# Kernel optimization log

Measured on AMD Instinct MI355X. Metric: run time of the kernel, lower is better.

Reference implementation:

```python
import jax, jax.numpy as jnp
import numpy as np

B, T, F, H, D1, D2, OUT = 8192, 90, 7, 128, 128, 64, 30


def _layernorm(x, g, b, eps=1e-5):
    mu = jnp.mean(x, axis=-1, keepdims=True)
    var = jnp.mean((x - mu) ** 2, axis=-1, keepdims=True)
    return (x - mu) * jax.lax.rsqrt(var + eps) * g + b


def _lstm_layer(x, Wih, Whh, bih, bhh):
    # x: [B,T,H_in]; Wih: [4H,H_in]; Whh: [4H,H]; biases [4H]. PyTorch gate order i,f,g,o.
    xg = jnp.einsum('bti,gi->btg', x, Wih) + bih + bhh  # [B,T,4H] precomputed input projection
    xg_t = jnp.swapaxes(xg, 0, 1)  # [T,B,4H]

    def step(carry, gx):
        h, c = carry
        gates = gx + h @ Whh.T  # [B,4H]
        i, f, g, o = jnp.split(gates, 4, axis=-1)
        c = jax.nn.sigmoid(f) * c + jax.nn.sigmoid(i) * jnp.tanh(g)
        h = jax.nn.sigmoid(o) * jnp.tanh(c)
        return (h, c), h

    h0 = jnp.zeros((x.shape[0], H), x.dtype)
    (_, _), hs = jax.lax.scan(step, (h0, h0), xg_t)
    return jnp.swapaxes(hs, 0, 1)  # [B,T,H]


def setup_inputs() -> dict:
    key = jax.random.key(0)
    ks = jax.random.split(key, 16)
    s = lambda k, shape, scale: jax.random.normal(k, shape, jnp.float32) * scale
    inp = {
        'x': s(ks[0], (B, T, F), 1.0),
        'W_in': s(ks[1], (H, F), 0.3), 'b_in': jnp.zeros((H,)),
        'g_in': jnp.ones((H,)), 'be_in': jnp.zeros((H,)),
        'Wih0': s(ks[2], (4 * H, H), 0.08), 'Whh0': s(ks[3], (4 * H, H), 0.08),
        'bih0': jnp.zeros((4 * H,)).at[H:2 * H].set(1.0), 'bhh0': jnp.zeros((4 * H,)),
        'Wih1': s(ks[4], (4 * H, H), 0.08), 'Whh1': s(ks[5], (4 * H, H), 0.08),
        'bih1': jnp.zeros((4 * H,)).at[H:2 * H].set(1.0), 'bhh1': jnp.zeros((4 * H,)),
        'g_ln': jnp.ones((H,)), 'be_ln': jnp.zeros((H,)),
        'W_d1': s(ks[6], (D1, H), 0.12), 'b_d1': jnp.zeros((D1,)),
        'W_d2': s(ks[7], (D2, D1), 0.12), 'b_d2': jnp.zeros((D2,)),
        'W_d3': s(ks[8], (OUT, D2), 0.15), 'b_d3': jnp.zeros((OUT,)),
    }
    return inp


def reference(x, W_in, b_in, g_in, be_in,
              Wih0, Whh0, bih0, bhh0, Wih1, Whh1, bih1, bhh1,
              g_ln, be_ln, W_d1, b_d1, W_d2, b_d2, W_d3, b_d3):
    h = _layernorm(jnp.einsum('btf,hf->bth', x, W_in) + b_in, g_in, be_in)
    h = _lstm_layer(h, Wih0, Whh0, bih0, bhh0)
    h = _lstm_layer(h, Wih1, Whh1, bih1, bhh1)  # dropout between layers is eval no-op
    last = _layernorm(h[:, -1, :], g_ln, be_ln)  # [B,H]
    d = jax.nn.relu(last @ W_d1.T + b_d1)
    d = jax.nn.relu(d @ W_d2.T + b_d2)
    return d @ W_d3.T + b_d3  # [B,30]
```

## Files before the change

### kernel.cpp

```cpp
#include <hip/hip_runtime.h>

#define DEV __device__ __forceinline__
typedef unsigned short u16;
typedef unsigned int u32;
typedef __bf16 bf16x8 __attribute__((ext_vector_type(8)));
typedef float f32x4 __attribute__((ext_vector_type(4)));

static constexpr int B = 8192, T = 90, F = 7, H = 128, NOUT = 30;

DEV float fexp2(float x) { return __builtin_amdgcn_exp2f(x); }
DEV float frcp(float x) { return __builtin_amdgcn_rcpf(x); }
DEV float frsq(float x) { return __builtin_amdgcn_rsqf(x); }
DEV float sigm(float x) { return frcp(1.f + fexp2(-1.44269504088896341f * x)); }
DEV u16 f2bfbits(float f) { __bf16 b = (__bf16)f; return __builtin_bit_cast(u16, b); }
DEV float bfbits2f(u32 u) { return __builtin_bit_cast(float, u << 16); }
DEV u32 pk2(float a, float b) { return (u32)f2bfbits(a) | ((u32)f2bfbits(b) << 16); }

DEV float wave_sum(float v) {
#pragma unroll
    for (int m = 32; m; m >>= 1) v += __shfl_xor(v, m, 64);
    return v;
}

__global__ __launch_bounds__(512) void prep_aux(
    const float* __restrict__ W_in, const float* __restrict__ b_in,
    const float* __restrict__ g_in, const float* __restrict__ be_in,
    const float* __restrict__ Wih0, float* __restrict__ aux, u16* __restrict__ Uhat) {
    const int tid = threadIdx.x;
    if (tid < 7) {
        float sm = 0.f, sp = 0.f;
        for (int h = 0; h < 128; ++h) { const float w = W_in[h * 7 + tid]; sm += w; sp += w * b_in[h]; }
        aux[tid] = sm * (1.f / 128.f); aux[64 + tid] = sp * (1.f / 128.f);
    } else if (tid < 56) {
        const int cd = tid - 7, cc = cd / 7, dd = cd % 7;
        float s = 0.f;
        for (int h = 0; h < 128; ++h) s += W_in[h * 7 + cc] * W_in[h * 7 + dd];
        aux[8 + cd] = s * (1.f / 128.f);
    } else if (tid == 56) {
        float s = 0.f; for (int h = 0; h < 128; ++h) s += b_in[h];
        aux[7] = s * (1.f / 128.f);
    } else if (tid == 57) {
        float s = 0.f; for (int h = 0; h < 128; ++h) s += b_in[h] * b_in[h];
        aux[72] = s * (1.f / 128.f);
    }
    float acc[10];
#pragma unroll
    for (int i = 0; i < 10; ++i) acc[i] = 0.f;
    const float* wr = Wih0 + (long)tid * 128;
    for (int h = 0; h < 128; ++h) {
        const float wv = wr[h], wg = wv * g_in[h];
#pragma unroll
        for (int cc = 0; cc < 7; ++cc) acc[cc] += wg * W_in[h * 7 + cc];
        acc[7] += wg * b_in[h]; acc[8] += wg; acc[9] += wv * be_in[h];
    }
    u16* dst = Uhat + tid * 32;
#pragma unroll
    for (int cc = 0; cc < 10; ++cc) dst[cc] = f2bfbits(acc[cc]);
#pragma unroll
    for (int cc = 10; cc < 32; ++cc) dst[cc] = 0;
}

__global__ __launch_bounds__(256) void prep_stats(
    const float* __restrict__ x, const float* __restrict__ aux,
    float2* __restrict__ stats) {
    __shared__ float sa[80];
    const int tid = threadIdx.x;
    if (tid < 80) sa[tid] = aux[tid];
    __syncthreads();
    const long idx = (long)blockIdx.x * 256 + tid;
    const float* xr = x + idx * 7;
    float xv[7];
#pragma unroll
    for (int cc = 0; cc < 7; ++cc) xv[cc] = xr[cc];
    float mu = sa[7];
#pragma unroll
    for (int cc = 0; cc < 7; ++cc) mu += sa[cc] * xv[cc];
    float q = sa[72];
#pragma unroll
    for (int cc = 0; cc < 7; ++cc) {
        float tacc = 2.f * sa[64 + cc];
#pragma unroll
        for (int dd = 0; dd < 7; ++dd) tacc += sa[8 + cc * 7 + dd] * xv[dd];
        q += xv[cc] * tacc;
    }
    const float rstd = frsq(q - mu * mu + 1e-5f);
    stats[idx] = make_float2(rstd, -rstd * mu);
}

__global__ __launch_bounds__(512, 2) void lstm_rec_l1(
    const float* __restrict__ x, const float2* __restrict__ stats,
    const u16* __restrict__ Uhat, const float* __restrict__ Whh,
    const float* __restrict__ bih, const float* __restrict__ bhh,
    u16* __restrict__ hs) {
    __shared__ __align__(16) u16 s_z[2][2][4][16][8];
    __shared__ __align__(16) u16 s_h[2][2][16 * 128];

    const int tid = threadIdx.x;
    const int wave = tid >> 6, lane = tid & 63, quad = lane >> 4, n16 = lane & 15;
    const int b0 = blockIdx.x * 32;

    for (int i = tid; i < 2 * 2 * 4 * 16 * 8; i += 512) ((u16*)s_z)[i] = 0;
    for (int i = tid; i < 2 * 16 * 128; i += 512) ((u16*)s_h[1])[i] = 0;

    bf16x8 bU[4], bWhh[4][4];
    float bias[4];
#pragma unroll
    for (int g = 0; g < 4; ++g) {
        const int wrow = g * 128 + 16 * wave + n16;
        bias[g] = bih[wrow] + bhh[wrow];
        bU[g] = *(const bf16x8*)&Uhat[wrow * 32 + quad * 8];
#pragma unroll
        for (int kk = 0; kk < 4; ++kk) {
            const float* ph = Whh + (long)wrow * 128 + kk * 32 + quad * 8;
            bf16x8 bh;
#pragma unroll
            for (int j = 0; j < 8; ++j) bh[j] = (__bf16)ph[j];
            bWhh[g][kk] = bh;
        }
    }

    const f32x4 zero4 = {0.f, 0.f, 0.f, 0.f};
    float c[2][4];
#pragma unroll
    for (int mt = 0; mt < 2; ++mt)
#pragma unroll
        for (int r = 0; r < 4; ++r) c[mt][r] = 0.f;

    const bool stager = (lane < 8);
    const int tau = wave * 8 + lane;
    const int srow = tau & 31, skk8 = tau >> 5;
    const int smt = srow >> 4, sm = srow & 15;
    const long srowg = (long)(b0 + srow) * T;

    const int ftile = tid >> 8, finner = tid & 255;
    const int fm = finner & 15, fkk8 = finner >> 4;
    const int fldsoff = (fkk8 * 16 + fm) * 8;
    const size_t fgrow = (size_t)(b0 + ftile * 16 + fm) * T;
    const int fgcol = fkk8 * 8;

    __syncthreads();

    if (stager) {
        const float2 st0 = stats[srowg];
        u32 p0, p1, p2, p3;
        if (skk8 == 0) {
            const float* xp = x + srowg * 7;
            const float rs = st0.x;
            p0 = pk2(rs * xp[0], rs * xp[1]); p1 = pk2(rs * xp[2], rs * xp[3]);
            p2 = pk2(rs * xp[4], rs * xp[5]); p3 = pk2(rs * xp[6], rs);
        } else { p0 = pk2(st0.y, 1.f); p1 = 0; p2 = 0; p3 = 0; }
        *(uint4*)&s_z[0][smt][skk8][sm][0] = (uint4){p0, p1, p2, p3};
    }
    __syncthreads();

#pragma unroll 1
    for (int t = 0; t < T; ++t) {
        const int par = t & 1;
        const int t1 = t + 1;
        const bool hasPre = stager && (t1 < T);
        float2 nst = {};
        float nx[7];
        if (hasPre) {
            nst = stats[srowg + t1];
            if (skk8 == 0) {
                const float* xp = x + (srowg + t1) * 7;
#pragma unroll
                for (int j = 0; j < 7; ++j) nx[j] = xp[j];
            }
        }
        if (t > 0) {
            const uint4 hv = *(const uint4*)&s_h[par ^ 1][ftile][fldsoff];
            *(uint4*)(hs + (fgrow + (t - 1)) * 128 + fgcol) = hv;
        }

#pragma unroll
        for (int mt = 0; mt < 2; ++mt) {
            const bf16x8 az = *(const bf16x8*)&s_z[par][mt][quad][n16][0];
            bf16x8 ah[4];
#pragma unroll
            for (int kk = 0; kk < 4; ++kk)
                ah[kk] = *(const bf16x8*)&s_h[par ^ 1][mt][((kk * 4 + quad) * 16 + n16) * 8];
            f32x4 acc[4];
#pragma unroll
            for (int g = 0; g < 4; ++g) {
                f32x4 a = __builtin_amdgcn_mfma_f32_16x16x32_bf16(az, bU[g], zero4, 0, 0, 0);
#pragma unroll
                for (int kk = 0; kk < 4; ++kk)
                    a = __builtin_amdgcn_mfma_f32_16x16x32_bf16(ah[kk], bWhh[g][kk], a, 0, 0, 0);
                acc[g] = a;
            }
#pragma unroll
            for (int r = 0; r < 4; ++r) {
                const float xi = acc[0][r] + bias[0];
                const float xf = acc[1][r] + bias[1];
                const float xg = acc[2][r] + bias[2];
                const float xo = acc[3][r] + bias[3];
                const float tg = 2.f * frcp(1.f + fexp2(-2.88539008177792681f * xg)) - 1.f;
                const float cn = sigm(xf) * c[mt][r] + sigm(xi) * tg;
                c[mt][r] = cn;
                const float so = sigm(xo);
                const float rr = frcp(1.f + fexp2(-2.88539008177792681f * cn));
                const float hv = __builtin_fmaf(2.f * so, rr, -so);
                s_h[par][mt][((2 * wave + (n16 >> 3)) * 16 + (quad * 4 + r)) * 8 + (n16 & 7)] =
                    f2bfbits(hv);
            }
        }

        if (hasPre) {
            u32 p0, p1, p2, p3;
            if (skk8 == 0) {
                const float rs = nst.x;
                p0 = pk2(rs * nx[0], rs * nx[1]); p1 = pk2(rs * nx[2], rs * nx[3]);
                p2 = pk2(rs * nx[4], rs * nx[5]); p3 = pk2(rs * nx[6], rs);
            } else { p0 = pk2(nst.y, 1.f); p1 = 0; p2 = 0; p3 = 0; }
            *(uint4*)&s_z[par ^ 1][smt][skk8][sm][0] = (uint4){p0, p1, p2, p3};
        }
        __syncthreads();
    }
    {
        const uint4 hv = *(const uint4*)&s_h[1][ftile][fldsoff];
        *(uint4*)(hs + (fgrow + (T - 1)) * 128 + fgcol) = hv;
    }
}

__global__ __launch_bounds__(512, 2) void lstm_rec_l2(
    const float* __restrict__ Wih, const float* __restrict__ Whh,
    const float* __restrict__ bih, const float* __restrict__ bhh,
    const u16* __restrict__ xin, u16* __restrict__ hlast) {
    __shared__ __align__(16) u16 s_x[2][2][16 * 128];
    __shared__ __align__(16) u16 s_h[2][2][16 * 128];

    const int tid = threadIdx.x;
    const int wave = tid >> 6, lane = tid & 63, quad = lane >> 4, n16 = lane & 15;
    const int b0 = blockIdx.x * 32;

    for (int i = tid; i < 2 * 16 * 128; i += 512) ((u16*)s_h[1])[i] = 0;

    bf16x8 bWih[4][4], bWhh[4][4];
    float bias[4];
#pragma unroll
    for (int g = 0; g < 4; ++g) {
        const int wrow = g * 128 + 16 * wave + n16;
        bias[g] = bih[wrow] + bhh[wrow];
#pragma unroll
        for (int kk = 0; kk < 4; ++kk) {
            const float* pi = Wih + (long)wrow * 128 + kk * 32 + quad * 8;
            const float* ph = Whh + (long)wrow * 128 + kk * 32 + quad * 8;
            bf16x8 bi, bh;
#pragma unroll
            for (int j = 0; j < 8; ++j) { bi[j] = (__bf16)pi[j]; bh[j] = (__bf16)ph[j]; }
            bWih[g][kk] = bi; bWhh[g][kk] = bh;
        }
    }

    const f32x4 zero4 = {0.f, 0.f, 0.f, 0.f};
    float c[2][4];
#pragma unroll
    for (int mt = 0; mt < 2; ++mt)
#pragma unroll
        for (int r = 0; r < 4; ++r) c[mt][r] = 0.f;

    const int stile = tid >> 8, sinner = tid & 255;
    const int sm = sinner & 15, skk8 = sinner >> 4;
    const u16* gsrc = xin + (size_t)(b0 + stile * 16 + sm) * T * 128 + skk8 * 8;
    const int ftile = tid >> 8, finner = tid & 255;
    const int fm = finner & 15, fkk8 = finner >> 4;
    const int fldsoff = (fkk8 * 16 + fm) * 8;
    const int fgcol = fkk8 * 8;

    {
        const uint4 v = *(const uint4*)gsrc;
        *(uint4*)&s_x[0][stile][sinner * 8] = v;
    }
    __syncthreads();

#pragma unroll 1
    for (int t = 0; t < T; ++t) {
        const int par = t & 1;
        uint4 pre = {};
        const bool hasPre = (t + 1 < T);
        if (hasPre) pre = *(const uint4*)(gsrc + (size_t)(t + 1) * 128);

#pragma unroll
        for (int mt = 0; mt < 2; ++mt) {
            bf16x8 aln[4], ah[4];
#pragma unroll
            for (int kk = 0; kk < 4; ++kk) {
                aln[kk] = *(const bf16x8*)&s_x[par][mt][((kk * 4 + quad) * 16 + n16) * 8];
                ah[kk] = *(const bf16x8*)&s_h[par ^ 1][mt][((kk * 4 + quad) * 16 + n16) * 8];
            }
            f32x4 acc[4];
#pragma unroll
            for (int g = 0; g < 4; ++g) {
                f32x4 a = __builtin_amdgcn_mfma_f32_16x16x32_bf16(aln[0], bWih[g][0], zero4, 0, 0, 0);
                a = __builtin_amdgcn_mfma_f32_16x16x32_bf16(ah[0], bWhh[g][0], a, 0, 0, 0);
#pragma unroll
                for (int kk = 1; kk < 4; ++kk) {
                    a = __builtin_amdgcn_mfma_f32_16x16x32_bf16(aln[kk], bWih[g][kk], a, 0, 0, 0);
                    a = __builtin_amdgcn_mfma_f32_16x16x32_bf16(ah[kk], bWhh[g][kk], a, 0, 0, 0);
                }
                acc[g] = a;
            }
#pragma unroll
            for (int r = 0; r < 4; ++r) {
                const float xi = acc[0][r] + bias[0];
                const float xf = acc[1][r] + bias[1];
                const float xg = acc[2][r] + bias[2];
                const float xo = acc[3][r] + bias[3];
                const float tg = 2.f * frcp(1.f + fexp2(-2.88539008177792681f * xg)) - 1.f;
                const float cn = sigm(xf) * c[mt][r] + sigm(xi) * tg;
                c[mt][r] = cn;
                const float so = sigm(xo);
                const float rr = frcp(1.f + fexp2(-2.88539008177792681f * cn));
                const float hv = __builtin_fmaf(2.f * so, rr, -so);
                s_h[par][mt][((2 * wave + (n16 >> 3)) * 16 + (quad * 4 + r)) * 8 + (n16 & 7)] =
                    f2bfbits(hv);
            }
        }
        if (hasPre) *(uint4*)&s_x[par ^ 1][stile][sinner * 8] = pre;
        __syncthreads();
    }
    {
        const uint4 hv = *(const uint4*)&s_h[1][ftile][fldsoff];
        *(uint4*)(hlast + (size_t)(b0 + ftile * 16 + fm) * 128 + fgcol) = hv;
    }
}

__global__ __launch_bounds__(256) void dense_head(
    const u16* __restrict__ hlast, const float* __restrict__ g_ln,
    const float* __restrict__ be_ln, const float* __restrict__ W_d1,
    const float* __restrict__ b_d1, const float* __restrict__ W_d2,
    const float* __restrict__ b_d2, const float* __restrict__ W_d3,
    const float* __restrict__ b_d3, float* __restrict__ out) {
    __shared__ float s_ln[16][128];
    __shared__ float s_d1[16][128];
    __shared__ float s_d2[16][64];
    const int wave = threadIdx.x >> 6, lane = threadIdx.x & 63;
    const long base = (long)blockIdx.x * 16;
    const int R = wave * 4;

#pragma unroll
    for (int rr = 0; rr < 4; ++rr) {
        const long row = base + R + rr;
        const u32 packed = ((const u32*)hlast)[row * 64 + lane];
        float v0 = bfbits2f(packed & 0xffffu), v1 = bfbits2f(packed >> 16);
        const float s = wave_sum(v0 + v1);
        const float q = wave_sum(v0 * v0 + v1 * v1);
        const float mu = s * (1.f / 128.f);
        const float rstd = frsq(q * (1.f / 128.f) - mu * mu + 1e-5f);
        const int h0 = 2 * lane;
        s_ln[R + rr][h0] = (v0 - mu) * rstd * g_ln[h0] + be_ln[h0];
        s_ln[R + rr][h0 + 1] = (v1 - mu) * rstd * g_ln[h0 + 1] + be_ln[h0 + 1];
    }
    __syncthreads();

#pragma unroll
    for (int half = 0; half < 2; ++half) {
        const int o = lane + 64 * half;
        float a[4] = {b_d1[o], b_d1[o], b_d1[o], b_d1[o]};
        const float4* wr = (const float4*)(W_d1 + (long)o * 128);
#pragma unroll 8
        for (int k = 0; k < 32; ++k) {
            const float4 wv = wr[k];
#pragma unroll
            for (int rr = 0; rr < 4; ++rr) {
                const float4 xv = ((const float4*)s_ln[R + rr])[k];
                a[rr] += wv.x * xv.x + wv.y * xv.y + wv.z * xv.z + wv.w * xv.w;
            }
        }
#pragma unroll
        for (int rr = 0; rr < 4; ++rr) s_d1[R + rr][o] = fmaxf(a[rr], 0.f);
    }
    __syncthreads();

    {
        float a[4] = {b_d2[lane], b_d2[lane], b_d2[lane], b_d2[lane]};
        const float4* wr = (const float4*)(W_d2 + (long)lane * 128);
#pragma unroll 8
        for (int k = 0; k < 32; ++k) {
            const float4 wv = wr[k];
#pragma unroll
            for (int rr = 0; rr < 4; ++rr) {
                const float4 xv = ((const float4*)s_d1[R + rr])[k];
                a[rr] += wv.x * xv.x + wv.y * xv.y + wv.z * xv.z + wv.w * xv.w;
            }
        }
#pragma unroll
        for (int rr = 0; rr < 4; ++rr) s_d2[R + rr][lane] = fmaxf(a[rr], 0.f);
    }
    __syncthreads();

    if (lane < NOUT) {
        float a[4] = {b_d3[lane], b_d3[lane], b_d3[lane], b_d3[lane]};
        const float4* wr = (const float4*)(W_d3 + (long)lane * 64);
#pragma unroll
        for (int k = 0; k < 16; ++k) {
            const float4 wv = wr[k];
#pragma unroll
            for (int rr = 0; rr < 4; ++rr) {
                const float4 xv = ((const float4*)s_d2[R + rr])[k];
                a[rr] += wv.x * xv.x + wv.y * xv.y + wv.z * xv.z + wv.w * xv.w;
            }
        }
#pragma unroll
        for (int rr = 0; rr < 4; ++rr) out[(base + R + rr) * NOUT + lane] = a[rr];
    }
}

extern "C" void kernel_launch(void* const* d_in, const int* in_sizes, int n_in,
                              void* d_out, int out_size, void* d_ws, size_t ws_size,
                              hipStream_t stream) {
    const float* x = (const float*)d_in[0];
    const float* W_in = (const float*)d_in[1];
    const float* b_in = (const float*)d_in[2];
    const float* g_in = (const float*)d_in[3];
    const float* be_in = (const float*)d_in[4];
    const float* Wih0 = (const float*)d_in[5];
    const float* Whh0 = (const float*)d_in[6];
    const float* bih0 = (const float*)d_in[7];
    const float* bhh0 = (const float*)d_in[8];
    const float* Wih1 = (const float*)d_in[9];
    const float* Whh1 = (const float*)d_in[10];
    const float* bih1 = (const float*)d_in[11];
    const float* bhh1 = (const float*)d_in[12];
    const float* g_ln = (const float*)d_in[13];
    const float* be_ln = (const float*)d_in[14];
    const float* W_d1 = (const float*)d_in[15];
    const float* b_d1 = (const float*)d_in[16];
    const float* W_d2 = (const float*)d_in[17];
    const float* b_d2 = (const float*)d_in[18];
    const float* W_d3 = (const float*)d_in[19];
    const float* b_d3 = (const float*)d_in[20];
    float* out = (float*)d_out;

    char* w = (char*)d_ws;
    float* aux = (float*)w;               w += 512;
    u16* Uhat = (u16*)w;                  w += 512 * 32 * sizeof(u16);
    float2* stats = (float2*)w;           w += (size_t)B * T * sizeof(float2);
    u16* hs0 = (u16*)w;                   w += (size_t)B * T * H * sizeof(u16);
    u16* hlast = (u16*)w;

    prep_aux<<<1, 512, 0, stream>>>(W_in, b_in, g_in, be_in, Wih0, aux, Uhat);
    prep_stats<<<(B * T) / 256, 256, 0, stream>>>(x, aux, stats);
    lstm_rec_l1<<<B / 32, 512, 0, stream>>>(x, stats, Uhat, Whh0, bih0, bhh0, hs0);
    lstm_rec_l2<<<B / 32, 512, 0, stream>>>(Wih1, Whh1, bih1, bhh1, hs0, hlast);
    dense_head<<<B / 16, 256, 0, stream>>>(hlast, g_ln, be_ln, W_d1, b_d1, W_d2, b_d2,
                                           W_d3, b_d3, out);
}
```

Measured before the change: 554.3 us.

## Interleave two batch tiles to overlap gate math with MFMA in LSTM recurrences

Both LSTM recurrence kernels now process the two 16-row batch tiles in a staggered way. The gate nonlinearities of one tile run while the MFMAs of the other tile issue, with a triple-buffered input stage and a barrier per half-step. The bias is folded into the MFMA accumulator init. A new cvt3 kernel pre-converts the recurrent and input weights to bf16 once, so each block no longer converts fp32 weights itself. The cost is one extra launch, more live registers under a 2-blocks-per-CU launch bound, and twice as many __syncthreads per timestep.

```diff
diff --git a/kernel.cpp b/kernel.cpp
--- a/kernel.cpp
+++ b/kernel.cpp
@@ -60,6 +60,18 @@
     for (int cc = 10; cc < 32; ++cc) dst[cc] = 0;
 }
 
+__global__ __launch_bounds__(256) void cvt3(
+    const float* __restrict__ a, const float* __restrict__ b,
+    const float* __restrict__ c, u16* __restrict__ dst) {
+    const long i = (long)blockIdx.x * 256 + threadIdx.x;
+    const int which = (int)(i >> 14);
+    const long off = (i & 16383) * 4;
+    const float* src = which == 0 ? a : (which == 1 ? b : c);
+    const float4 v = *(const float4*)(src + off);
+    u32 p0 = pk2(v.x, v.y), p1 = pk2(v.z, v.w);
+    *(uint2*)(dst + (long)which * 65536 + off) = (uint2){p0, p1};
+}
+
 __global__ __launch_bounds__(256) void prep_stats(
     const float* __restrict__ x, const float* __restrict__ aux,
     float2* __restrict__ stats) {
@@ -89,240 +101,243 @@
 
 __global__ __launch_bounds__(512, 2) void lstm_rec_l1(
     const float* __restrict__ x, const float2* __restrict__ stats,
-    const u16* __restrict__ Uhat, const float* __restrict__ Whh,
+    const u16* __restrict__ Uhat, const u16* __restrict__ Whhb,
     const float* __restrict__ bih, const float* __restrict__ bhh,
     u16* __restrict__ hs) {
-    __shared__ __align__(16) u16 s_z[2][2][4][16][8];
-    __shared__ __align__(16) u16 s_h[2][2][16 * 128];
+    __shared__ __align__(16) u16 s_z[2][3][4][16][8];
+    __shared__ __align__(16) u16 s_h[2][2][2048];
 
     const int tid = threadIdx.x;
     const int wave = tid >> 6, lane = tid & 63, quad = lane >> 4, n16 = lane & 15;
     const int b0 = blockIdx.x * 32;
 
-    for (int i = tid; i < 2 * 2 * 4 * 16 * 8; i += 512) ((u16*)s_z)[i] = 0;
-    for (int i = tid; i < 2 * 16 * 128; i += 512) ((u16*)s_h[1])[i] = 0;
+    for (int i = tid; i < 2 * 3 * 4 * 16 * 8; i += 512) ((u16*)s_z)[i] = 0;
+    for (int i = tid; i < 2048; i += 512) { s_h[0][1][i] = 0; s_h[1][1][i] = 0; }
 
     bf16x8 bU[4], bWhh[4][4];
-    float bias[4];
+    f32x4 bias4[4];
 #pragma unroll
     for (int g = 0; g < 4; ++g) {
         const int wrow = g * 128 + 16 * wave + n16;
-        bias[g] = bih[wrow] + bhh[wrow];
+        const float bb = bih[wrow] + bhh[wrow];
+        bias4[g] = (f32x4){bb, bb, bb, bb};
         bU[g] = *(const bf16x8*)&Uhat[wrow * 32 + quad * 8];
 #pragma unroll
-        for (int kk = 0; kk < 4; ++kk) {
-            const float* ph = Whh + (long)wrow * 128 + kk * 32 + quad * 8;
-            bf16x8 bh;
-#pragma unroll
-            for (int j = 0; j < 8; ++j) bh[j] = (__bf16)ph[j];
-            bWhh[g][kk] = bh;
-        }
-    }
-
-    const f32x4 zero4 = {0.f, 0.f, 0.f, 0.f};
-    float c[2][4];
-#pragma unroll
-    for (int mt = 0; mt < 2; ++mt)
-#pragma unroll
-        for (int r = 0; r < 4; ++r) c[mt][r] = 0.f;
-
-    const bool stager = (lane < 8);
-    const int tau = wave * 8 + lane;
-    const int srow = tau & 31, skk8 = tau >> 5;
-    const int smt = srow >> 4, sm = srow & 15;
-    const long srowg = (long)(b0 + srow) * T;
-
-    const int ftile = tid >> 8, finner = tid & 255;
-    const int fm = finner & 15, fkk8 = finner >> 4;
-    const int fldsoff = (fkk8 * 16 + fm) * 8;
-    const size_t fgrow = (size_t)(b0 + ftile * 16 + fm) * T;
-    const int fgcol = fkk8 * 8;
-
-    __syncthreads();
-
-    if (stager) {
-        const float2 st0 = stats[srowg];
+        for (int kk = 0; kk < 4; ++kk)
+            bWhh[g][kk] = *(const bf16x8*)&Whhb[(long)wrow * 128 + kk * 32 + quad * 8];
+    }
+
+    const bool zst = (tid < 32);
+    const int srow = tid & 15, skk8z = tid >> 4;
+    const bool stg = (tid < 256);
+    const int fm = tid & 15, fkk8 = (tid >> 4) & 15;
+    const int fldso = (fkk8 * 16 + fm) * 8;
+
+    auto build_z = [&](size_t sidx, u16* dst) {
+        const float2 st = stats[sidx];
         u32 p0, p1, p2, p3;
-        if (skk8 == 0) {
-            const float* xp = x + srowg * 7;
-            const float rs = st0.x;
+        if (skk8z == 0) {
+            const float* xp = x + sidx * 7;
+            const float rs = st.x;
             p0 = pk2(rs * xp[0], rs * xp[1]); p1 = pk2(rs * xp[2], rs * xp[3]);
             p2 = pk2(rs * xp[4], rs * xp[5]); p3 = pk2(rs * xp[6], rs);
-        } else { p0 = pk2(st0.y, 1.f); p1 = 0; p2 = 0; p3 = 0; }
-        *(uint4*)&s_z[0][smt][skk8][sm][0] = (uint4){p0, p1, p2, p3};
-    }
-    __syncthreads();
+        } else { p0 = pk2(st.y, 1.f); p1 = 0; p2 = 0; p3 = 0; }
+        *(uint4*)dst = (uint4){p0, p1, p2, p3};
+    };
+
+    __syncthreads();
+
+    if (zst) {
+#pragma unroll
+        for (int tl = 0; tl < 2; ++tl)
+#pragma unroll
+            for (int tt = 0; tt < 2; ++tt)
+                build_z((size_t)(b0 + tl * 16 + srow) * T + tt, &s_z[tl][tt][skk8z][srow][0]);
+    }
+    __syncthreads();
+
+    auto do_mfma = [&](const u16* szb, const u16* shb, f32x4* gcn) {
+        const bf16x8 az = *(const bf16x8*)&szb[(quad * 16 + n16) * 8];
+        bf16x8 ah[4];
+#pragma unroll
+        for (int kk = 0; kk < 4; ++kk)
+            ah[kk] = *(const bf16x8*)&shb[((kk * 4 + quad) * 16 + n16) * 8];
+#pragma unroll
+        for (int g = 0; g < 4; ++g) {
+            f32x4 a = __builtin_amdgcn_mfma_f32_16x16x32_bf16(az, bU[g], bias4[g], 0, 0, 0);
+#pragma unroll
+            for (int kk = 0; kk < 4; ++kk)
+                a = __builtin_amdgcn_mfma_f32_16x16x32_bf16(ah[kk], bWhh[g][kk], a, 0, 0, 0);
+            gcn[g] = a;
+        }
+    };
+    auto do_gates = [&](const f32x4* gco, float* cc, u16* shout) {
+#pragma unroll
+        for (int r = 0; r < 4; ++r) {
+            const float xi = gco[0][r], xf = gco[1][r], xgg = gco[2][r], xo = gco[3][r];
+            const float tg = 2.f * frcp(1.f + fexp2(-2.88539008177792681f * xgg)) - 1.f;
+            const float cn = sigm(xf) * cc[r] + sigm(xi) * tg;
+            cc[r] = cn;
+            const float so = sigm(xo);
+            const float rr = frcp(1.f + fexp2(-2.88539008177792681f * cn));
+            const float hv = __builtin_fmaf(2.f * so, rr, -so);
+            shout[((2 * wave + (n16 >> 3)) * 16 + (quad * 4 + r)) * 8 + (n16 & 7)] = f2bfbits(hv);
+        }
+    };
+
+    float cA[4] = {0.f, 0.f, 0.f, 0.f}, cB[4] = {0.f, 0.f, 0.f, 0.f};
+    f32x4 gc[4], gn[4];
 
 #pragma unroll 1
-    for (int t = 0; t < T; ++t) {
-        const int par = t & 1;
-        const int t1 = t + 1;
-        const bool hasPre = stager && (t1 < T);
-        float2 nst = {};
-        float nx[7];
-        if (hasPre) {
-            nst = stats[srowg + t1];
-            if (skk8 == 0) {
-                const float* xp = x + (srowg + t1) * 7;
-#pragma unroll
-                for (int j = 0; j < 7; ++j) nx[j] = xp[j];
-            }
-        }
-        if (t > 0) {
-            const uint4 hv = *(const uint4*)&s_h[par ^ 1][ftile][fldsoff];
-            *(uint4*)(hs + (fgrow + (t - 1)) * 128 + fgcol) = hv;
-        }
-
-#pragma unroll
-        for (int mt = 0; mt < 2; ++mt) {
-            const bf16x8 az = *(const bf16x8*)&s_z[par][mt][quad][n16][0];
-            bf16x8 ah[4];
-#pragma unroll
-            for (int kk = 0; kk < 4; ++kk)
-                ah[kk] = *(const bf16x8*)&s_h[par ^ 1][mt][((kk * 4 + quad) * 16 + n16) * 8];
-            f32x4 acc[4];
-#pragma unroll
-            for (int g = 0; g < 4; ++g) {
-                f32x4 a = __builtin_amdgcn_mfma_f32_16x16x32_bf16(az, bU[g], zero4, 0, 0, 0);
-#pragma unroll
-                for (int kk = 0; kk < 4; ++kk)
-                    a = __builtin_amdgcn_mfma_f32_16x16x32_bf16(ah[kk], bWhh[g][kk], a, 0, 0, 0);
-                acc[g] = a;
-            }
-#pragma unroll
-            for (int r = 0; r < 4; ++r) {
-                const float xi = acc[0][r] + bias[0];
-                const float xf = acc[1][r] + bias[1];
-                const float xg = acc[2][r] + bias[2];
-                const float xo = acc[3][r] + bias[3];
-                const float tg = 2.f * frcp(1.f + fexp2(-2.88539008177792681f * xg)) - 1.f;
-                const float cn = sigm(xf) * c[mt][r] + sigm(xi) * tg;
-                c[mt][r] = cn;
-                const float so = sigm(xo);
-                const float rr = frcp(1.f + fexp2(-2.88539008177792681f * cn));
-                const float hv = __builtin_fmaf(2.f * so, rr, -so);
-                s_h[par][mt][((2 * wave + (n16 >> 3)) * 16 + (quad * 4 + r)) * 8 + (n16 & 7)] =
-                    f2bfbits(hv);
-            }
-        }
-
-        if (hasPre) {
-            u32 p0, p1, p2, p3;
-            if (skk8 == 0) {
-                const float rs = nst.x;
-                p0 = pk2(rs * nx[0], rs * nx[1]); p1 = pk2(rs * nx[2], rs * nx[3]);
-                p2 = pk2(rs * nx[4], rs * nx[5]); p3 = pk2(rs * nx[6], rs);
-            } else { p0 = pk2(nst.y, 1.f); p1 = 0; p2 = 0; p3 = 0; }
-            *(uint4*)&s_z[par ^ 1][smt][skk8][sm][0] = (uint4){p0, p1, p2, p3};
-        }
+    for (int t2 = 0; t2 < T; ++t2) {
+        const int tm = t2 % 3;
+        const int tw = (tm >= 1) ? tm - 1 : tm + 2;
+        const int ph = t2 & 1, pho = ph ^ 1;
+        const bool hasPre = (t2 + 2 < T);
+
+        do_mfma(&s_z[0][tm][0][0][0], s_h[0][pho], gn);
+        if (t2 > 0 && stg) {
+            const uint4 hv = *(const uint4*)&s_h[0][pho][fldso];
+            *(uint4*)(hs + ((size_t)(b0 + fm) * T + (t2 - 1)) * 128 + fkk8 * 8) = hv;
+        }
+        if (t2 > 0) do_gates(gc, cB, s_h[1][pho]);
+#pragma unroll
+        for (int g = 0; g < 4; ++g) gc[g] = gn[g];
+        if (hasPre && zst)
+            build_z((size_t)(b0 + srow) * T + t2 + 2, &s_z[0][tw][skk8z][srow][0]);
         __syncthreads();
-    }
-    {
-        const uint4 hv = *(const uint4*)&s_h[1][ftile][fldsoff];
-        *(uint4*)(hs + (fgrow + (T - 1)) * 128 + fgcol) = hv;
+
+        do_mfma(&s_z[1][tm][0][0][0], s_h[1][pho], gn);
+        if (t2 > 0 && stg) {
+            const uint4 hv = *(const uint4*)&s_h[1][pho][fldso];
+            *(uint4*)(hs + ((size_t)(b0 + 16 + fm) * T + (t2 - 1)) * 128 + fkk8 * 8) = hv;
+        }
+        do_gates(gc, cA, s_h[0][ph]);
+#pragma unroll
+        for (int g = 0; g < 4; ++g) gc[g] = gn[g];
+        if (hasPre && zst)
+            build_z((size_t)(b0 + 16 + srow) * T + t2 + 2, &s_z[1][tw][skk8z][srow][0]);
+        __syncthreads();
+    }
+    do_gates(gc, cB, s_h[1][1]);
+    __syncthreads();
+    if (stg) {
+        const uint4 hvA = *(const uint4*)&s_h[0][1][fldso];
+        const uint4 hvB = *(const uint4*)&s_h[1][1][fldso];
+        *(uint4*)(hs + ((size_t)(b0 + fm) * T + (T - 1)) * 128 + fkk8 * 8) = hvA;
+        *(uint4*)(hs + ((size_t)(b0 + 16 + fm) * T + (T - 1)) * 128 + fkk8 * 8) = hvB;
     }
 }
 
 __global__ __launch_bounds__(512, 2) void lstm_rec_l2(
-    const float* __restrict__ Wih, const float* __restrict__ Whh,
+    const u16* __restrict__ Wihb, const u16* __restrict__ Whhb,
     const float* __restrict__ bih, const float* __restrict__ bhh,
     const u16* __restrict__ xin, u16* __restrict__ hlast) {
-    __shared__ __align__(16) u16 s_x[2][2][16 * 128];
-    __shared__ __align__(16) u16 s_h[2][2][16 * 128];
+    __shared__ __align__(16) u16 s_x[2][3][2048];
+    __shared__ __align__(16) u16 s_h[2][2][2048];
 
     const int tid = threadIdx.x;
     const int wave = tid >> 6, lane = tid & 63, quad = lane >> 4, n16 = lane & 15;
     const int b0 = blockIdx.x * 32;
 
-    for (int i = tid; i < 2 * 16 * 128; i += 512) ((u16*)s_h[1])[i] = 0;
+    for (int i = tid; i < 2048; i += 512) { s_h[0][1][i] = 0; s_h[1][1][i] = 0; }
 
     bf16x8 bWih[4][4], bWhh[4][4];
-    float bias[4];
+    f32x4 bias4[4];
 #pragma unroll
     for (int g = 0; g < 4; ++g) {
         const int wrow = g * 128 + 16 * wave + n16;
-        bias[g] = bih[wrow] + bhh[wrow];
+        const float bb = bih[wrow] + bhh[wrow];
+        bias4[g] = (f32x4){bb, bb, bb, bb};
 #pragma unroll
         for (int kk = 0; kk < 4; ++kk) {
-            const float* pi = Wih + (long)wrow * 128 + kk * 32 + quad * 8;
-            const float* ph = Whh + (long)wrow * 128 + kk * 32 + quad * 8;
-            bf16x8 bi, bh;
-#pragma unroll
-            for (int j = 0; j < 8; ++j) { bi[j] = (__bf16)pi[j]; bh[j] = (__bf16)ph[j]; }
-            bWih[g][kk] = bi; bWhh[g][kk] = bh;
-        }
-    }
-
-    const f32x4 zero4 = {0.f, 0.f, 0.f, 0.f};
-    float c[2][4];
-#pragma unroll
-    for (int mt = 0; mt < 2; ++mt)
-#pragma unroll
-        for (int r = 0; r < 4; ++r) c[mt][r] = 0.f;
-
-    const int stile = tid >> 8, sinner = tid & 255;
-    const int sm = sinner & 15, skk8 = sinner >> 4;
-    const u16* gsrc = xin + (size_t)(b0 + stile * 16 + sm) * T * 128 + skk8 * 8;
-    const int ftile = tid >> 8, finner = tid & 255;
-    const int fm = finner & 15, fkk8 = finner >> 4;
-    const int fldsoff = (fkk8 * 16 + fm) * 8;
-    const int fgcol = fkk8 * 8;
-
-    {
-        const uint4 v = *(const uint4*)gsrc;
-        *(uint4*)&s_x[0][stile][sinner * 8] = v;
-    }
-    __syncthreads();
+            bWih[g][kk] = *(const bf16x8*)&Wihb[(long)wrow * 128 + kk * 32 + quad * 8];
+            bWhh[g][kk] = *(const bf16x8*)&Whhb[(long)wrow * 128 + kk * 32 + quad * 8];
+        }
+    }
+
+    const bool stg = (tid < 256);
+    const int fm = tid & 15, fkk8 = (tid >> 4) & 15;
+    const int fldso = (fkk8 * 16 + fm) * 8;
+    const u16* gsA = xin + (size_t)(b0 + fm) * T * 128 + fkk8 * 8;
+    const u16* gsB = xin + (size_t)(b0 + 16 + fm) * T * 128 + fkk8 * 8;
+
+    if (stg) {
+#pragma unroll
+        for (int tt = 0; tt < 2; ++tt) {
+            *(uint4*)&s_x[0][tt][fldso] = *(const uint4*)(gsA + (size_t)tt * 128);
+            *(uint4*)&s_x[1][tt][fldso] = *(const uint4*)(gsB + (size_t)tt * 128);
+        }
+    }
+    __syncthreads();
+
+    auto do_mfma = [&](const u16* sxb, const u16* shb, f32x4* gcn) {
+        bf16x8 ax[4], ah[4];
+#pragma unroll
+        for (int kk = 0; kk < 4; ++kk) {
+            ax[kk] = *(const bf16x8*)&sxb[((kk * 4 + quad) * 16 + n16) * 8];
+            ah[kk] = *(const bf16x8*)&shb[((kk * 4 + quad) * 16 + n16) * 8];
+        }
+#pragma unroll
+        for (int g = 0; g < 4; ++g) {
+            f32x4 a = bias4[g];
+#pragma unroll
+            for (int kk = 0; kk < 4; ++kk) {
+                a = __builtin_amdgcn_mfma_f32_16x16x32_bf16(ax[kk], bWih[g][kk], a, 0, 0, 0);
+                a = __builtin_amdgcn_mfma_f32_16x16x32_bf16(ah[kk], bWhh[g][kk], a, 0, 0, 0);
+            }
+            gcn[g] = a;
+        }
+    };
+    auto do_gates = [&](const f32x4* gco, float* cc, u16* shout) {
+#pragma unroll
+        for (int r = 0; r < 4; ++r) {
+            const float xi = gco[0][r], xf = gco[1][r], xgg = gco[2][r], xo = gco[3][r];
+            const float tg = 2.f * frcp(1.f + fexp2(-2.88539008177792681f * xgg)) - 1.f;
+            const float cn = sigm(xf) * cc[r] + sigm(xi) * tg;
+            cc[r] = cn;
+            const float so = sigm(xo);
+            const float rr = frcp(1.f + fexp2(-2.88539008177792681f * cn));
+            const float hv = __builtin_fmaf(2.f * so, rr, -so);
+            shout[((2 * wave + (n16 >> 3)) * 16 + (quad * 4 + r)) * 8 + (n16 & 7)] = f2bfbits(hv);
+        }
+    };
+
+    float cA[4] = {0.f, 0.f, 0.f, 0.f}, cB[4] = {0.f, 0.f, 0.f, 0.f};
+    f32x4 gc[4], gn[4];
 
 #pragma unroll 1
-    for (int t = 0; t < T; ++t) {
-        const int par = t & 1;
-        uint4 pre = {};
-        const bool hasPre = (t + 1 < T);
-        if (hasPre) pre = *(const uint4*)(gsrc + (size_t)(t + 1) * 128);
-
-#pragma unroll
-        for (int mt = 0; mt < 2; ++mt) {
-            bf16x8 aln[4], ah[4];
-#pragma unroll
-            for (int kk = 0; kk < 4; ++kk) {
-                aln[kk] = *(const bf16x8*)&s_x[par][mt][((kk * 4 + quad) * 16 + n16) * 8];
-                ah[kk] = *(const bf16x8*)&s_h[par ^ 1][mt][((kk * 4 + quad) * 16 + n16) * 8];
-            }
-            f32x4 acc[4];
-#pragma unroll
-            for (int g = 0; g < 4; ++g) {
-                f32x4 a = __builtin_amdgcn_mfma_f32_16x16x32_bf16(aln[0], bWih[g][0], zero4, 0, 0, 0);
-                a = __builtin_amdgcn_mfma_f32_16x16x32_bf16(ah[0], bWhh[g][0], a, 0, 0, 0);
-#pragma unroll
-                for (int kk = 1; kk < 4; ++kk) {
-                    a = __builtin_amdgcn_mfma_f32_16x16x32_bf16(aln[kk], bWih[g][kk], a, 0, 0, 0);
-                    a = __builtin_amdgcn_mfma_f32_16x16x32_bf16(ah[kk], bWhh[g][kk], a, 0, 0, 0);
-                }
-                acc[g] = a;
-            }
-#pragma unroll
-            for (int r = 0; r < 4; ++r) {
-                const float xi = acc[0][r] + bias[0];
-                const float xf = acc[1][r] + bias[1];
-                const float xg = acc[2][r] + bias[2];
-                const float xo = acc[3][r] + bias[3];
-                const float tg = 2.f * frcp(1.f + fexp2(-2.88539008177792681f * xg)) - 1.f;
-                const float cn = sigm(xf) * c[mt][r] + sigm(xi) * tg;
-                c[mt][r] = cn;
-                const float so = sigm(xo);
-                const float rr = frcp(1.f + fexp2(-2.88539008177792681f * cn));
-                const float hv = __builtin_fmaf(2.f * so, rr, -so);
-                s_h[par][mt][((2 * wave + (n16 >> 3)) * 16 + (quad * 4 + r)) * 8 + (n16 & 7)] =
-                    f2bfbits(hv);
-            }
-        }
-        if (hasPre) *(uint4*)&s_x[par ^ 1][stile][sinner * 8] = pre;
+    for (int t2 = 0; t2 < T; ++t2) {
+        const int tm = t2 % 3;
+        const int tw = (tm >= 1) ? tm - 1 : tm + 2;
+        const int ph = t2 & 1, pho = ph ^ 1;
+        const bool hasPre = (t2 + 2 < T);
+
+        uint4 preA = {};
+        if (hasPre && stg) preA = *(const uint4*)(gsA + (size_t)(t2 + 2) * 128);
+        do_mfma(s_x[0][tm], s_h[0][pho], gn);
+        if (t2 > 0) do_gates(gc, cB, s_h[1][pho]);
+#pragma unroll
+        for (int g = 0; g < 4; ++g) gc[g] = gn[g];
+        if (hasPre && stg) *(uint4*)&s_x[0][tw][fldso] = preA;
         __syncthreads();
-    }
-    {
-        const uint4 hv = *(const uint4*)&s_h[1][ftile][fldsoff];
-        *(uint4*)(hlast + (size_t)(b0 + ftile * 16 + fm) * 128 + fgcol) = hv;
+
+        uint4 preB = {};
+        if (hasPre && stg) preB = *(const uint4*)(gsB + (size_t)(t2 + 2) * 128);
+        do_mfma(s_x[1][tm], s_h[1][pho], gn);
+        do_gates(gc, cA, s_h[0][ph]);
+#pragma unroll
+        for (int g = 0; g < 4; ++g) gc[g] = gn[g];
+        if (hasPre && stg) *(uint4*)&s_x[1][tw][fldso] = preB;
+        __syncthreads();
+    }
+    do_gates(gc, cB, s_h[1][1]);
+    __syncthreads();
+    if (stg) {
+        const uint4 hvA = *(const uint4*)&s_h[0][1][fldso];
+        const uint4 hvB = *(const uint4*)&s_h[1][1][fldso];
+        *(uint4*)(hlast + (size_t)(b0 + fm) * 128 + fkk8 * 8) = hvA;
+        *(uint4*)(hlast + (size_t)(b0 + 16 + fm) * 128 + fkk8 * 8) = hvB;
     }
 }
 
@@ -436,14 +451,19 @@
     char* w = (char*)d_ws;
     float* aux = (float*)w;               w += 512;
     u16* Uhat = (u16*)w;                  w += 512 * 32 * sizeof(u16);
+    u16* wb = (u16*)w;                    w += 3 * 512 * 128 * sizeof(u16);
     float2* stats = (float2*)w;           w += (size_t)B * T * sizeof(float2);
     u16* hs0 = (u16*)w;                   w += (size_t)B * T * H * sizeof(u16);
     u16* hlast = (u16*)w;
+    u16* Whh0b = wb;
+    u16* Wih1b = wb + 65536;
+    u16* Whh1b = wb + 131072;
 
     prep_aux<<<1, 512, 0, stream>>>(W_in, b_in, g_in, be_in, Wih0, aux, Uhat);
+    cvt3<<<192, 256, 0, stream>>>(Whh0, Wih1, Whh1, wb);
     prep_stats<<<(B * T) / 256, 256, 0, stream>>>(x, aux, stats);
-    lstm_rec_l1<<<B / 32, 512, 0, stream>>>(x, stats, Uhat, Whh0, bih0, bhh0, hs0);
-    lstm_rec_l2<<<B / 32, 512, 0, stream>>>(Wih1, Whh1, bih1, bhh1, hs0, hlast);
+    lstm_rec_l1<<<B / 32, 512, 0, stream>>>(x, stats, Uhat, Whh0b, bih0, bhh0, hs0);
+    lstm_rec_l2<<<B / 32, 512, 0, stream>>>(Wih1b, Whh1b, bih1, bhh1, hs0, hlast);
     dense_head<<<B / 16, 256, 0, stream>>>(hlast, g_ln, be_ln, W_d1, b_d1, W_d2, b_d2,
                                            W_d3, b_d3, out);
 }
```

Result: slower. 567.5 us (+2.4%).
